# Optimization experiments

Measured on AMD Instinct MI355X. Metric: run time of the kernel, lower is better.

## Reference

```python
import jax, jax.numpy as jnp
import numpy as np

NUM_ANGLES = 360
IMAGE_SIZE = 256
BATCH = 8


def _radon_forward(x, num_angles=NUM_ANGLES):
    # x: [B, 1, D, D]; replicates torch affine_grid + grid_sample(bilinear,
    # padding_mode='zeros', align_corners=False) followed by mean over rows.
    B = x.shape[0]
    D = x.shape[-1]
    img = x[:, 0]  # [B, D, D]
    angles = jnp.linspace(0.0, 180.0, num_angles + 1, dtype=x.dtype)[:-1]
    t = jnp.deg2rad(angles)
    c, s = jnp.cos(t), jnp.sin(t)
    # align_corners=False normalized pixel-center coords in [-1, 1]
    coords = (2.0 * jnp.arange(D, dtype=x.dtype) + 1.0) / D - 1.0
    xw = coords[None, None, :]   # output x (width)
    yh = coords[None, :, None]   # output y (height)
    cN = c[:, None, None]
    sN = s[:, None, None]
    # theta = [[c, -s, 0], [s, c, 0]] applied to (x_out, y_out, 1)
    gx = cN * xw - sN * yh       # [A, D, D]
    gy = sN * xw + cN * yh
    # unnormalize (align_corners=False)
    ix = ((gx + 1.0) * D - 1.0) * 0.5
    iy = ((gy + 1.0) * D - 1.0) * 0.5
    x0 = jnp.floor(ix)
    y0 = jnp.floor(iy)
    x1 = x0 + 1.0
    y1 = y0 + 1.0
    wx1 = ix - x0
    wx0 = 1.0 - wx1
    wy1 = iy - y0
    wy0 = 1.0 - wy1
    img_flat = img.reshape(B, D * D)

    def corner(xc, yc, w):
        valid = (xc >= 0) & (xc <= D - 1) & (yc >= 0) & (yc <= D - 1)
        xi = jnp.clip(xc, 0, D - 1).astype(jnp.int32)
        yi = jnp.clip(yc, 0, D - 1).astype(jnp.int32)
        lin = yi * D + xi                      # [A, D, D]
        vals = img_flat[:, lin]                # [B, A, D, D]
        return vals * (w * valid.astype(x.dtype))[None]

    rotated = (corner(x0, y0, wx0 * wy0) + corner(x1, y0, wx1 * wy0)
               + corner(x0, y1, wx0 * wy1) + corner(x1, y1, wx1 * wy1))
    proj = rotated.mean(axis=2)                # mean over rows (H) -> [B, A, D]
    return proj[:, None]                       # [B, 1, A, D]


def setup_inputs() -> dict:
    key = jax.random.key(0)
    x = jax.random.normal(key, (BATCH, 1, IMAGE_SIZE, IMAGE_SIZE), dtype=jnp.float32)
    return {"x": x}


def reference(x) -> jnp.ndarray:
    return _radon_forward(x)
```

## Files before the change

### kernel.cpp

```cpp
#include <hip/hip_runtime.h>

#define DD 256
#define BB 8
#define NA 360

typedef _Float16 half2_t __attribute__((ext_vector_type(2)));

#if defined(__has_builtin)
#if __has_builtin(__builtin_elementwise_fma)
#define PKFMA(a, b, c) __builtin_elementwise_fma((a), (b), (c))
#endif
#endif
#ifndef PKFMA
#define PKFMA(a, b, c) ((a) * (b) + (c))
#endif

__device__ __forceinline__ half2_t h2(unsigned u) {
    return __builtin_bit_cast(half2_t, u);
}
__device__ __forceinline__ half2_t bcast2(float w) {
    return __builtin_bit_cast(half2_t, __builtin_amdgcn_cvt_pkrtz(w, w));
}
__device__ __forceinline__ unsigned pk_f16(float a, float b) {
    unsigned short ua = __builtin_bit_cast(unsigned short, (_Float16)a);
    unsigned short ub = __builtin_bit_cast(unsigned short, (_Float16)b);
    return (unsigned)ua | ((unsigned)ub << 16);
}

__global__ __launch_bounds__(256) void pack_f16(const float* __restrict__ x,
                                                uint4* __restrict__ pN,
                                                uint4* __restrict__ pT) {
    __shared__ uint4 t[32][33];
    const int tx = threadIdx.x & 31;
    const int ty = threadIdx.x >> 5;
    const int x0 = (blockIdx.x & 7) * 32;
    const int y0 = (blockIdx.x >> 3) * 32;

#pragma unroll
    for (int r = ty; r < 32; r += 8) {
        const int pix = (y0 + r) * DD + x0 + tx;
        uint4 v;
        v.x = pk_f16(x[0 * DD * DD + pix], x[1 * DD * DD + pix]);
        v.y = pk_f16(x[2 * DD * DD + pix], x[3 * DD * DD + pix]);
        v.z = pk_f16(x[4 * DD * DD + pix], x[5 * DD * DD + pix]);
        v.w = pk_f16(x[6 * DD * DD + pix], x[7 * DD * DD + pix]);
        pN[pix] = v;
        t[r][tx] = v;
    }
    __syncthreads();
#pragma unroll
    for (int r = ty; r < 32; r += 8)
        pT[(x0 + r) * DD + y0 + tx] = t[tx][r];
}

__global__ __launch_bounds__(256) void radon_pk(const uint4* __restrict__ pN,
                                                const uint4* __restrict__ pT,
                                                float* __restrict__ out) {
    const int a    = blockIdx.x;
    const int wseg = blockIdx.y;
    const int g    = threadIdx.x >> 6;
    const int lane = threadIdx.x & 63;
    const int w    = wseg * 64 + lane;

    const float ang = (float)a * 0.5f;
    const float t = ang * 0.017453292519943295f;
    const float s = sinf(t);
    const float c = cosf(t);

    const float uw  = (float)w - 127.5f;
    const float axN = fmaf(c, uw, 127.5f);
    const float ayN = fmaf(s, uw, 127.5f);

    const uint4* __restrict__ P;
    float ax, dx, ay, dy;
    if (fabsf(s) <= fabsf(c)) { P = pN; ax = axN; dx = -s; ay = ayN; dy = c;  }
    else                      { P = pT; ax = ayN; dx = c;  ay = axN; dy = -s; }

    half2_t acc2[4];
#pragma unroll
    for (int j = 0; j < 4; ++j) acc2[j] = half2_t{(_Float16)0, (_Float16)0};

#pragma unroll 4
    for (int i = 0; i < 64; ++i) {
        const float uh = (float)(g + 4 * i) - 127.5f;
        const float ix = fmaf(dx, uh, ax);
        const float iy = fmaf(dy, uh, ay);
        const float x0f = floorf(ix), y0f = floorf(iy);
        const float wx1 = ix - x0f, wy1 = iy - y0f;
        const float wx0 = 1.f - wx1, wy0 = 1.f - wy1;
        const int x0 = (int)x0f, y0 = (int)y0f;
        const float vx0 = ((unsigned)x0 < 256u) ? wx0 : 0.f;
        const float vx1 = ((unsigned)(x0 + 1) < 256u) ? wx1 : 0.f;
        const float vy0 = ((unsigned)y0 < 256u) ? wy0 : 0.f;
        const float vy1 = ((unsigned)(y0 + 1) < 256u) ? wy1 : 0.f;
        const int x0c = min(max(x0, 0), 255);
        const int x1c = min(max(x0 + 1, 0), 255);
        const int y0c = min(max(y0, 0), 255);
        const int y1c = min(max(y0 + 1, 0), 255);

        const uint4 q00 = P[y0c * DD + x0c];
        const uint4 q10 = P[y0c * DD + x1c];
        const uint4 q01 = P[y1c * DD + x0c];
        const uint4 q11 = P[y1c * DD + x1c];

        const half2_t w00 = bcast2(vx0 * vy0);
        const half2_t w10 = bcast2(vx1 * vy0);
        const half2_t w01 = bcast2(vx0 * vy1);
        const half2_t w11 = bcast2(vx1 * vy1);

        acc2[0] = PKFMA(h2(q00.x), w00, acc2[0]);
        acc2[1] = PKFMA(h2(q00.y), w00, acc2[1]);
        acc2[2] = PKFMA(h2(q00.z), w00, acc2[2]);
        acc2[3] = PKFMA(h2(q00.w), w00, acc2[3]);
        acc2[0] = PKFMA(h2(q10.x), w10, acc2[0]);
        acc2[1] = PKFMA(h2(q10.y), w10, acc2[1]);
        acc2[2] = PKFMA(h2(q10.z), w10, acc2[2]);
        acc2[3] = PKFMA(h2(q10.w), w10, acc2[3]);
        acc2[0] = PKFMA(h2(q01.x), w01, acc2[0]);
        acc2[1] = PKFMA(h2(q01.y), w01, acc2[1]);
        acc2[2] = PKFMA(h2(q01.z), w01, acc2[2]);
        acc2[3] = PKFMA(h2(q01.w), w01, acc2[3]);
        acc2[0] = PKFMA(h2(q11.x), w11, acc2[0]);
        acc2[1] = PKFMA(h2(q11.y), w11, acc2[1]);
        acc2[2] = PKFMA(h2(q11.z), w11, acc2[2]);
        acc2[3] = PKFMA(h2(q11.w), w11, acc2[3]);
    }

    float acc[BB];
#pragma unroll
    for (int j = 0; j < 4; ++j) {
        acc[2 * j]     = (float)acc2[j].x;
        acc[2 * j + 1] = (float)acc2[j].y;
    }

    __shared__ float part[4][64][BB];
#pragma unroll
    for (int b = 0; b < BB; b += 4)
        *(float4*)&part[g][lane][b] = make_float4(acc[b], acc[b + 1], acc[b + 2], acc[b + 3]);
    __syncthreads();

    const float sc = 1.0f / 256.0f;
#pragma unroll
    for (int k = 0; k < 2; ++k) {
        const int id = threadIdx.x + k * 256;
        const int b  = id >> 6;
        const int wl = id & 63;
        const float v = part[0][wl][b] + part[1][wl][b] + part[2][wl][b] + part[3][wl][b];
        out[(size_t)b * NA * DD + (size_t)a * DD + wseg * 64 + wl] = v * sc;
    }
}

__global__ __launch_bounds__(256) void radon_direct(const float* __restrict__ x,
                                                    float* __restrict__ out) {
    const int a  = blockIdx.x;
    const int hc = blockIdx.y;
    const int w  = threadIdx.x;
    const float ang = (float)a * 0.5f;
    const float t = ang * 0.017453292519943295f;
    const float s = sinf(t);
    const float c = cosf(t);
    const float uw = (float)w - 127.5f;
    const float ax = fmaf(c, uw, 127.5f);
    const float ay = fmaf(s, uw, 127.5f);

    float acc[BB];
#pragma unroll
    for (int b = 0; b < BB; ++b) acc[b] = 0.f;

    const int h0 = hc * 32;
    for (int i = 0; i < 32; ++i) {
        const float uh = (float)(h0 + i) - 127.5f;
        const float ix = fmaf(-s, uh, ax);
        const float iy = fmaf(c, uh, ay);
        const float x0f = floorf(ix), y0f = floorf(iy);
        const float wx1 = ix - x0f, wy1 = iy - y0f;
        const float wx0 = 1.f - wx1, wy0 = 1.f - wy1;
        const int x0 = (int)x0f, y0 = (int)y0f;
        const float vx0 = ((unsigned)x0 < 256u) ? wx0 : 0.f;
        const float vx1 = ((unsigned)(x0 + 1) < 256u) ? wx1 : 0.f;
        const float vy0 = ((unsigned)y0 < 256u) ? wy0 : 0.f;
        const float vy1 = ((unsigned)(y0 + 1) < 256u) ? wy1 : 0.f;
        const int x0c = min(max(x0, 0), 255);
        const int x1c = min(max(x0 + 1, 0), 255);
        const int y0c = min(max(y0, 0), 255);
        const int y1c = min(max(y0 + 1, 0), 255);
        const float w00 = vx0 * vy0, w10 = vx1 * vy0;
        const float w01 = vx0 * vy1, w11 = vx1 * vy1;
        const int l00 = y0c * DD + x0c, l10 = y0c * DD + x1c;
        const int l01 = y1c * DD + x0c, l11 = y1c * DD + x1c;
#pragma unroll
        for (int b = 0; b < BB; ++b) {
            const float* ib = x + (size_t)b * DD * DD;
            acc[b] = fmaf(ib[l00], w00, acc[b]);
            acc[b] = fmaf(ib[l10], w10, acc[b]);
            acc[b] = fmaf(ib[l01], w01, acc[b]);
            acc[b] = fmaf(ib[l11], w11, acc[b]);
        }
    }

    const float sc = 1.0f / 256.0f;
    float* o = out + (size_t)a * DD + w;
#pragma unroll
    for (int b = 0; b < BB; ++b)
        atomicAdd(o + (size_t)b * NA * DD, acc[b] * sc);
}

extern "C" void kernel_launch(void* const* d_in, const int* in_sizes, int n_in,
                              void* d_out, int out_size, void* d_ws, size_t ws_size,
                              hipStream_t stream) {
    const float* x = (const float*)d_in[0];
    float* out = (float*)d_out;

    const size_t need = 2ull * DD * DD * sizeof(uint4);
    if (ws_size >= need) {
        uint4* pN = (uint4*)d_ws;
        uint4* pT = pN + (size_t)DD * DD;
        pack_f16<<<64, 256, 0, stream>>>(x, pN, pT);
        radon_pk<<<dim3(NA, 4), 256, 0, stream>>>(pN, pT, out);
    } else {
        (void)hipMemsetAsync(d_out, 0, (size_t)out_size * sizeof(float), stream);
        radon_direct<<<dim3(NA, 8), 256, 0, stream>>>(x, out);
    }
}
```

Before: 126.1 us.

## Fuse pack and radon kernels with a global atomic counter barrier

Merges the f16 packing/transpose kernel into the radon kernel. The first 256 blocks pack 16x16 tiles and bump a device-scope counter, and every block spins until all 256 tiles are done before sampling. This removes one kernel launch and the inter-kernel gap, at the cost of a memset and a spin-wait grid barrier. That barrier relies on the first 256 blocks being resident or scheduled, which is a deadlock risk if later blocks occupy the GPU first.

New measurement: 162.0 us. 1.28x slower.

```diff
diff --git a/kernel.cpp b/kernel.cpp
--- a/kernel.cpp
+++ b/kernel.cpp
@@ -27,39 +27,46 @@
     return (unsigned)ua | ((unsigned)ub << 16);
 }
 
-__global__ __launch_bounds__(256) void pack_f16(const float* __restrict__ x,
-                                                uint4* __restrict__ pN,
-                                                uint4* __restrict__ pT) {
-    __shared__ uint4 t[32][33];
-    const int tx = threadIdx.x & 31;
-    const int ty = threadIdx.x >> 5;
-    const int x0 = (blockIdx.x & 7) * 32;
-    const int y0 = (blockIdx.x >> 3) * 32;
-
-#pragma unroll
-    for (int r = ty; r < 32; r += 8) {
-        const int pix = (y0 + r) * DD + x0 + tx;
+__global__ __launch_bounds__(256) void radon_fused(const float* __restrict__ x,
+                                                   uint4* __restrict__ pN,
+                                                   uint4* __restrict__ pT,
+                                                   unsigned* __restrict__ cnt,
+                                                   float* __restrict__ out) {
+    __shared__ uint4 tile[16][17];
+    __shared__ float part[4][64][BB];
+
+    const int bx  = blockIdx.x;
+    const int tid = threadIdx.x;
+
+    if (bx < 256) {
+        const int tx = tid & 15, ty = tid >> 4;
+        const int px0 = (bx & 15) * 16, py0 = (bx >> 4) * 16;
+        const int pix = (py0 + ty) * DD + px0 + tx;
         uint4 v;
         v.x = pk_f16(x[0 * DD * DD + pix], x[1 * DD * DD + pix]);
         v.y = pk_f16(x[2 * DD * DD + pix], x[3 * DD * DD + pix]);
         v.z = pk_f16(x[4 * DD * DD + pix], x[5 * DD * DD + pix]);
         v.w = pk_f16(x[6 * DD * DD + pix], x[7 * DD * DD + pix]);
         pN[pix] = v;
-        t[r][tx] = v;
+        tile[ty][tx] = v;
+        __syncthreads();
+        pT[(px0 + ty) * DD + py0 + tx] = tile[tx][ty];
+        __syncthreads();
+        if (tid == 0)
+            __hip_atomic_fetch_add(cnt, 1u, __ATOMIC_RELEASE, __HIP_MEMORY_SCOPE_AGENT);
+    }
+
+    if (tid == 0) {
+        while (__hip_atomic_load(cnt, __ATOMIC_RELAXED, __HIP_MEMORY_SCOPE_AGENT) < 256u)
+            __builtin_amdgcn_s_sleep(4);
+        __atomic_thread_fence(__ATOMIC_ACQUIRE);
     }
     __syncthreads();
-#pragma unroll
-    for (int r = ty; r < 32; r += 8)
-        pT[(x0 + r) * DD + y0 + tx] = t[tx][r];
-}
-
-__global__ __launch_bounds__(256) void radon_pk(const uint4* __restrict__ pN,
-                                                const uint4* __restrict__ pT,
-                                                float* __restrict__ out) {
-    const int a    = blockIdx.x;
-    const int wseg = blockIdx.y;
-    const int g    = threadIdx.x >> 6;
-    const int lane = threadIdx.x & 63;
+
+    const int a    = bx >> 2;
+    const int wseg = bx & 3;
+    const int g    = tid >> 6;
+    const int lane = tid & 63;
     const int w    = wseg * 64 + lane;
 
     const float ang = (float)a * 0.5f;
@@ -133,7 +140,6 @@
         acc[2 * j + 1] = (float)acc2[j].y;
     }
 
-    __shared__ float part[4][64][BB];
 #pragma unroll
     for (int b = 0; b < BB; b += 4)
         *(float4*)&part[g][lane][b] = make_float4(acc[b], acc[b + 1], acc[b + 2], acc[b + 3]);
@@ -142,7 +148,7 @@
     const float sc = 1.0f / 256.0f;
 #pragma unroll
     for (int k = 0; k < 2; ++k) {
-        const int id = threadIdx.x + k * 256;
+        const int id = tid + k * 256;
         const int b  = id >> 6;
         const int wl = id & 63;
         const float v = part[0][wl][b] + part[1][wl][b] + part[2][wl][b] + part[3][wl][b];
@@ -211,12 +217,13 @@
     const float* x = (const float*)d_in[0];
     float* out = (float*)d_out;
 
-    const size_t need = 2ull * DD * DD * sizeof(uint4);
+    const size_t need = (2ull << 20) + 64;
     if (ws_size >= need) {
         uint4* pN = (uint4*)d_ws;
         uint4* pT = pN + (size_t)DD * DD;
-        pack_f16<<<64, 256, 0, stream>>>(x, pN, pT);
-        radon_pk<<<dim3(NA, 4), 256, 0, stream>>>(pN, pT, out);
+        unsigned* cnt = (unsigned*)((char*)d_ws + (2ull << 20));
+        (void)hipMemsetAsync(cnt, 0, sizeof(unsigned), stream);
+        radon_fused<<<NA * 4, 256, 0, stream>>>(x, pN, pT, cnt, out);
     } else {
         (void)hipMemsetAsync(d_out, 0, (size_t)out_size * sizeof(float), stream);
         radon_direct<<<dim3(NA, 8), 256, 0, stream>>>(x, out);
```

## Tile output into 32x32 blocks with LDS-staged rotated source window

Applied to the files above, without the earlier changes.

Replaces the per-angle column kernel with 32x32 output tiles per angle. Each tile computes the bounding box of its rotated footprint, loads that window of packed fp16 pixels into LDS, and gathers bilinear samples from LDS instead of global memory. This drops the transposed copy of the image, and partial sums are combined with atomicAdd, which requires a memset of the output. The goal is to replace scattered global gathers with shared-memory reads, at the cost of many more blocks, window-load overhead, and atomics.

Measured after the change: 160.8 us. 1.27x slower.

```diff
diff --git a/kernel.cpp b/kernel.cpp
--- a/kernel.cpp
+++ b/kernel.cpp
@@ -3,6 +3,10 @@
 #define DD 256
 #define BB 8
 #define NA 360
+#define WT 32
+#define HT 32
+#define MAXC 46
+#define WSTR 47
 
 typedef _Float16 half2_t __attribute__((ext_vector_type(2)));
 
@@ -28,63 +32,80 @@
 }
 
 __global__ __launch_bounds__(256) void pack_f16(const float* __restrict__ x,
-                                                uint4* __restrict__ pN,
-                                                uint4* __restrict__ pT) {
-    __shared__ uint4 t[32][33];
-    const int tx = threadIdx.x & 31;
-    const int ty = threadIdx.x >> 5;
-    const int x0 = (blockIdx.x & 7) * 32;
-    const int y0 = (blockIdx.x >> 3) * 32;
-
-#pragma unroll
-    for (int r = ty; r < 32; r += 8) {
-        const int pix = (y0 + r) * DD + x0 + tx;
-        uint4 v;
-        v.x = pk_f16(x[0 * DD * DD + pix], x[1 * DD * DD + pix]);
-        v.y = pk_f16(x[2 * DD * DD + pix], x[3 * DD * DD + pix]);
-        v.z = pk_f16(x[4 * DD * DD + pix], x[5 * DD * DD + pix]);
-        v.w = pk_f16(x[6 * DD * DD + pix], x[7 * DD * DD + pix]);
-        pN[pix] = v;
-        t[r][tx] = v;
-    }
-    __syncthreads();
-#pragma unroll
-    for (int r = ty; r < 32; r += 8)
-        pT[(x0 + r) * DD + y0 + tx] = t[tx][r];
-}
-
-__global__ __launch_bounds__(256) void radon_pk(const uint4* __restrict__ pN,
-                                                const uint4* __restrict__ pT,
-                                                float* __restrict__ out) {
-    const int a    = blockIdx.x;
-    const int wseg = blockIdx.y;
-    const int g    = threadIdx.x >> 6;
-    const int lane = threadIdx.x & 63;
-    const int w    = wseg * 64 + lane;
+                                                uint4* __restrict__ pN) {
+    const int pix = blockIdx.x * 256 + threadIdx.x;
+    uint4 v;
+    v.x = pk_f16(x[0 * DD * DD + pix], x[1 * DD * DD + pix]);
+    v.y = pk_f16(x[2 * DD * DD + pix], x[3 * DD * DD + pix]);
+    v.z = pk_f16(x[4 * DD * DD + pix], x[5 * DD * DD + pix]);
+    v.w = pk_f16(x[6 * DD * DD + pix], x[7 * DD * DD + pix]);
+    pN[pix] = v;
+}
+
+__global__ __launch_bounds__(256) void radon_lds(const uint4* __restrict__ pN,
+                                                 float* __restrict__ out) {
+    __shared__ __align__(16) unsigned char smem[MAXC * WSTR * 16];
+    uint4* win = (uint4*)smem;
+
+    const int a   = blockIdx.x;
+    const int wt  = blockIdx.y & 7;
+    const int ht  = blockIdx.y >> 3;
+    const int tid = threadIdx.x;
 
     const float ang = (float)a * 0.5f;
     const float t = ang * 0.017453292519943295f;
     const float s = sinf(t);
     const float c = cosf(t);
 
-    const float uw  = (float)w - 127.5f;
-    const float axN = fmaf(c, uw, 127.5f);
-    const float ayN = fmaf(s, uw, 127.5f);
-
-    const uint4* __restrict__ P;
-    float ax, dx, ay, dy;
-    if (fabsf(s) <= fabsf(c)) { P = pN; ax = axN; dx = -s; ay = ayN; dy = c;  }
-    else                      { P = pT; ax = ayN; dx = c;  ay = axN; dy = -s; }
+    const int w0 = wt * WT, h0 = ht * HT;
+
+    float fxmin = 1e30f, fxmax = -1e30f, fymin = 1e30f, fymax = -1e30f;
+#pragma unroll
+    for (int i = 0; i < 4; ++i) {
+        const float uwc = (float)(w0 + (i & 1) * (WT - 1)) - 127.5f;
+        const float uhc = (float)(h0 + (i >> 1) * (HT - 1)) - 127.5f;
+        const float axc = fmaf(c, uwc, 127.5f);
+        const float ayc = fmaf(s, uwc, 127.5f);
+        const float ixc = fmaf(-s, uhc, axc);
+        const float iyc = fmaf(c, uhc, ayc);
+        fxmin = fminf(fxmin, ixc); fxmax = fmaxf(fxmax, ixc);
+        fymin = fminf(fymin, iyc); fymax = fmaxf(fymax, iyc);
+    }
+    const int x_lo = min(max((int)floorf(fxmin), 0), 255);
+    const int x_hi = min(max((int)floorf(fxmax) + 1, 0), 255);
+    const int y_lo = min(max((int)floorf(fymin), 0), 255);
+    const int y_hi = min(max((int)floorf(fymax) + 1, 0), 255);
+    const int ncols = x_hi - x_lo + 1;
+    const int nrows = y_hi - y_lo + 1;
+
+    {
+        const int cl = tid & 63;
+        const int r0 = tid >> 6;
+        for (int r = r0; r < nrows; r += 4)
+            if (cl < ncols)
+                win[r * WSTR + cl] = pN[(y_lo + r) * DD + x_lo + cl];
+    }
+    __syncthreads();
+
+    const int g    = tid >> 6;
+    const int lane = tid & 63;
+    const int hp   = lane >> 5;
+    const int wl   = lane & 31;
+
+    const float uw = (float)(w0 + wl) - 127.5f;
+    const float ax = fmaf(c, uw, 127.5f);
+    const float ay = fmaf(s, uw, 127.5f);
 
     half2_t acc2[4];
 #pragma unroll
     for (int j = 0; j < 4; ++j) acc2[j] = half2_t{(_Float16)0, (_Float16)0};
 
-#pragma unroll 4
-    for (int i = 0; i < 64; ++i) {
-        const float uh = (float)(g + 4 * i) - 127.5f;
-        const float ix = fmaf(dx, uh, ax);
-        const float iy = fmaf(dy, uh, ay);
+#pragma unroll
+    for (int k = 0; k < 4; ++k) {
+        const int h = h0 + 2 * g + hp + 8 * k;
+        const float uh = (float)h - 127.5f;
+        const float ix = fmaf(-s, uh, ax);
+        const float iy = fmaf(c, uh, ay);
         const float x0f = floorf(ix), y0f = floorf(iy);
         const float wx1 = ix - x0f, wy1 = iy - y0f;
         const float wx0 = 1.f - wx1, wy0 = 1.f - wy1;
@@ -93,15 +114,15 @@
         const float vx1 = ((unsigned)(x0 + 1) < 256u) ? wx1 : 0.f;
         const float vy0 = ((unsigned)y0 < 256u) ? wy0 : 0.f;
         const float vy1 = ((unsigned)(y0 + 1) < 256u) ? wy1 : 0.f;
-        const int x0c = min(max(x0, 0), 255);
-        const int x1c = min(max(x0 + 1, 0), 255);
-        const int y0c = min(max(y0, 0), 255);
-        const int y1c = min(max(y0 + 1, 0), 255);
-
-        const uint4 q00 = P[y0c * DD + x0c];
-        const uint4 q10 = P[y0c * DD + x1c];
-        const uint4 q01 = P[y1c * DD + x0c];
-        const uint4 q11 = P[y1c * DD + x1c];
+        const int rx0 = min(max(x0, 0), 255) - x_lo;
+        const int rx1 = min(max(x0 + 1, 0), 255) - x_lo;
+        const int ry0 = min(max(y0, 0), 255) - y_lo;
+        const int ry1 = min(max(y0 + 1, 0), 255) - y_lo;
+
+        const uint4 q00 = win[ry0 * WSTR + rx0];
+        const uint4 q10 = win[ry0 * WSTR + rx1];
+        const uint4 q01 = win[ry1 * WSTR + rx0];
+        const uint4 q11 = win[ry1 * WSTR + rx1];
 
         const half2_t w00 = bcast2(vx0 * vy0);
         const half2_t w10 = bcast2(vx1 * vy0);
@@ -133,21 +154,21 @@
         acc[2 * j + 1] = (float)acc2[j].y;
     }
 
-    __shared__ float part[4][64][BB];
+    __syncthreads();
+    float* part = (float*)smem;
+    const int p = g * 2 + hp;
 #pragma unroll
     for (int b = 0; b < BB; b += 4)
-        *(float4*)&part[g][lane][b] = make_float4(acc[b], acc[b + 1], acc[b + 2], acc[b + 3]);
+        *(float4*)&part[(p * 32 + wl) * BB + b] =
+            make_float4(acc[b], acc[b + 1], acc[b + 2], acc[b + 3]);
     __syncthreads();
 
     const float sc = 1.0f / 256.0f;
-#pragma unroll
-    for (int k = 0; k < 2; ++k) {
-        const int id = threadIdx.x + k * 256;
-        const int b  = id >> 6;
-        const int wl = id & 63;
-        const float v = part[0][wl][b] + part[1][wl][b] + part[2][wl][b] + part[3][wl][b];
-        out[(size_t)b * NA * DD + (size_t)a * DD + wseg * 64 + wl] = v * sc;
-    }
+    const int wl2 = tid & 31, b2 = tid >> 5;
+    float v = 0.f;
+#pragma unroll
+    for (int p2 = 0; p2 < 8; ++p2) v += part[(p2 * 32 + wl2) * BB + b2];
+    atomicAdd(out + (size_t)b2 * NA * DD + (size_t)a * DD + w0 + wl2, v * sc);
 }
 
 __global__ __launch_bounds__(256) void radon_direct(const float* __restrict__ x,
@@ -211,14 +232,14 @@
     const float* x = (const float*)d_in[0];
     float* out = (float*)d_out;
 
-    const size_t need = 2ull * DD * DD * sizeof(uint4);
+    (void)hipMemsetAsync(d_out, 0, (size_t)out_size * sizeof(float), stream);
+
+    const size_t need = (size_t)DD * DD * sizeof(uint4);
     if (ws_size >= need) {
         uint4* pN = (uint4*)d_ws;
-        uint4* pT = pN + (size_t)DD * DD;
-        pack_f16<<<64, 256, 0, stream>>>(x, pN, pT);
-        radon_pk<<<dim3(NA, 4), 256, 0, stream>>>(pN, pT, out);
+        pack_f16<<<DD * DD / 256, 256, 0, stream>>>(x, pN);
+        radon_lds<<<dim3(NA, 64), 256, 0, stream>>>(pN, out);
     } else {
-        (void)hipMemsetAsync(d_out, 0, (size_t)out_size * sizeof(float), stream);
         radon_direct<<<dim3(NA, 8), 256, 0, stream>>>(x, out);
     }
 }
```
